# Optimization experiments

Hardware: AMD Instinct MI355X
Metric: run time of the kernel (lower is better)

Reference implementation:

```python
import jax, jax.numpy as jnp
import numpy as np

# Module config (init_kwargs)
OUT_H, OUT_W = 7, 7
SPATIAL_SCALE = 0.25
SAMPLE_NUM = 2          # fixed sampling grid (sample_num > 0 branch of mmcv kernel)
ALIGNED = True
CLOCKWISE = False

B, C, H, W = 2, 256, 200, 200
R = 1000


def setup_inputs() -> dict:
    key = jax.random.key(0)
    k1, k2, k3, k4, k5, k6 = jax.random.split(key, 6)
    features = jax.random.normal(k1, (B, C, H, W), dtype=jnp.float32)
    # rois: (batch_index, cx, cy, w, h, angle) in input-image coordinates
    bidx = jax.random.randint(k2, (R,), 0, B).astype(jnp.float32)
    cx = jax.random.uniform(k3, (R,), minval=100.0, maxval=700.0)
    cy = jax.random.uniform(k4, (R,), minval=100.0, maxval=700.0)
    wh = jax.random.uniform(k5, (R, 2), minval=20.0, maxval=200.0)
    ang = jax.random.uniform(k6, (R,), minval=-np.pi, maxval=np.pi)
    rois = jnp.concatenate(
        [bidx[:, None], cx[:, None], cy[:, None], wh, ang[:, None]], axis=1
    ).astype(jnp.float32)
    return {"features": features, "rois": rois}


def _bilinear_gather(features, bidx, y, x):
    """features: [B,C,H,W]; bidx: [R] int; y,x: [R,P] float. Returns [R,P,C]."""
    Hf, Wf = features.shape[2], features.shape[3]
    valid = (y > -1.0) & (y < Hf) & (x > -1.0) & (x < Wf)
    y = jnp.maximum(y, 0.0)
    x = jnp.maximum(x, 0.0)
    yl = jnp.floor(y).astype(jnp.int32)
    xl = jnp.floor(x).astype(jnp.int32)
    ych = yl >= Hf - 1
    xch = xl >= Wf - 1
    yl = jnp.where(ych, Hf - 1, yl)
    yh = jnp.where(ych, Hf - 1, yl + 1)
    xl = jnp.where(xch, Wf - 1, xl)
    xh = jnp.where(xch, Wf - 1, xl + 1)
    ly = jnp.where(ych, 0.0, y - yl.astype(y.dtype))
    lx = jnp.where(xch, 0.0, x - xl.astype(x.dtype))
    hy, hx = 1.0 - ly, 1.0 - lx
    b = bidx[:, None]  # [R,1] broadcast against [R,P]
    v1 = features[b, :, yl, xl]  # [R,P,C]
    v2 = features[b, :, yl, xh]
    v3 = features[b, :, yh, xl]
    v4 = features[b, :, yh, xh]
    val = (hy * hx)[..., None] * v1 + (hy * lx)[..., None] * v2 \
        + (ly * hx)[..., None] * v3 + (ly * lx)[..., None] * v4
    return jnp.where(valid[..., None], val, 0.0)


def _roi_align_rotated(features, rois):
    g = SAMPLE_NUM
    offset = 0.5 if ALIGNED else 0.0
    bidx = rois[:, 0].astype(jnp.int32)
    cx = rois[:, 1] * SPATIAL_SCALE - offset
    cy = rois[:, 2] * SPATIAL_SCALE - offset
    rw = rois[:, 3] * SPATIAL_SCALE
    rh = rois[:, 4] * SPATIAL_SCALE
    theta = -rois[:, 5] if CLOCKWISE else rois[:, 5]
    if not ALIGNED:
        rw = jnp.maximum(rw, 1.0)
        rh = jnp.maximum(rh, 1.0)
    bin_h = rh / OUT_H
    bin_w = rw / OUT_W
    # sample offsets within roi frame, origin at roi center
    ph = jnp.arange(OUT_H, dtype=jnp.float32)
    pw = jnp.arange(OUT_W, dtype=jnp.float32)
    ig = (jnp.arange(g, dtype=jnp.float32) + 0.5) / g
    # yy: [R, OUT_H, g]; xx: [R, OUT_W, g]
    yy = -rh[:, None, None] / 2.0 + (ph[None, :, None] + ig[None, None, :]) * bin_h[:, None, None]
    xx = -rw[:, None, None] / 2.0 + (pw[None, :, None] + ig[None, None, :]) * bin_w[:, None, None]
    # broadcast to [R, OUT_H, OUT_W, g, g]
    yy5 = yy[:, :, None, :, None]
    xx5 = xx[:, None, :, None, :]
    sin_t = jnp.sin(theta)[:, None, None, None, None]
    cos_t = jnp.cos(theta)[:, None, None, None, None]
    x = yy5 * sin_t + xx5 * cos_t + cx[:, None, None, None, None]
    y = yy5 * cos_t - xx5 * sin_t + cy[:, None, None, None, None]
    P = OUT_H * OUT_W * g * g
    vals = _bilinear_gather(features, bidx, y.reshape(R, P), x.reshape(R, P))  # [R,P,C]
    vals = vals.reshape(R, OUT_H, OUT_W, g * g, C).mean(axis=3)  # [R,OUT_H,OUT_W,C]
    return jnp.transpose(vals, (0, 3, 1, 2))  # [R,C,OUT_H,OUT_W]


def reference(features, rois):
    return _roi_align_rotated(features, rois)
```

## Files before the change

kernel.cpp:

```cpp
#include <hip/hip_runtime.h>
#include <math.h>

#define OUT_H 7
#define OUT_W 7
#define GS 2
#define NBINS (OUT_H * OUT_W)
#define NSAMP (GS * GS)
#define NMETA (NBINS * NSAMP)
#define SPATIAL_SCALE 0.25f
#define B_ 2
#define C_ 256
#define H_ 200
#define W_ 200
#define R_ 1000
#define HW_ (H_ * W_)

typedef _Float16 half_t;
typedef __attribute__((ext_vector_type(8))) _Float16 half8;
typedef __attribute__((ext_vector_type(2))) _Float16 half2_t;
typedef __attribute__((ext_vector_type(4))) float f32x4;


__global__ __launch_bounds__(256)
void nchw_to_nhwc_h(const float* __restrict__ in, half_t* __restrict__ out,
                    const float* __restrict__ rois, int* __restrict__ perm) {
    __shared__ float tile[64][64];

    __shared__ int bpos[8][64];
    __shared__ int novf, take;
    __shared__ unsigned char claimed[R_];
    __shared__ short ovf[R_];
    if (blockIdx.x == 0 && blockIdx.y == 0 && blockIdx.z == 0) {
        const int t0 = threadIdx.x;
        for (int i = t0; i < 8 * 64; i += 256) ((int*)bpos)[i] = 0;
        if (t0 == 0) { novf = 0; take = 0; }
        for (int t = t0; t < R_; t += 256) claimed[t] = 0;
        __syncthreads();
        for (int t = t0; t < R_; t += 256) {
            const float* roi = rois + t * 6;
            int   b   = (int)roi[0];
            float cyf = roi[2] * SPATIAL_SCALE;
            float cxf = roi[1] * SPATIAL_SCALE;
            int q = (int)((cyf - 25.0f) * (4.0f / 150.0f));
            q = q < 0 ? 0 : (q > 3 ? 3 : q);
            int band = b * 4 + q;
            band = band < 0 ? 0 : (band > 7 ? 7 : band);
            int bk = (int)((cxf - 25.0f) * (64.0f / 150.0f));
            bk = bk < 0 ? 0 : (bk > 63 ? 63 : bk);
            atomicAdd(&bpos[band][bk], 1);
        }
        __syncthreads();
        if (t0 < 8) {
            int s = 0;
            for (int k = 0; k < 64; ++k) {
                int c = bpos[t0][k];
                bpos[t0][k] = s;
                s += c;
            }
        }
        __syncthreads();
        for (int t = t0; t < R_; t += 256) {
            const float* roi = rois + t * 6;
            int   b   = (int)roi[0];
            float cyf = roi[2] * SPATIAL_SCALE;
            float cxf = roi[1] * SPATIAL_SCALE;
            int q = (int)((cyf - 25.0f) * (4.0f / 150.0f));
            q = q < 0 ? 0 : (q > 3 ? 3 : q);
            int band = b * 4 + q;
            band = band < 0 ? 0 : (band > 7 ? 7 : band);
            int bk = (int)((cxf - 25.0f) * (64.0f / 150.0f));
            bk = bk < 0 ? 0 : (bk > 63 ? 63 : bk);
            int pos = atomicAdd(&bpos[band][bk], 1);
            if (pos < R_ / 8) {
                int id = band + 8 * pos;
                perm[id] = t;
                claimed[id] = 1;
            } else {
                ovf[atomicAdd(&novf, 1)] = (short)t;
            }
        }
        __syncthreads();
        for (int t = t0; t < R_; t += 256) {
            if (!claimed[t]) perm[t] = (int)ovf[atomicAdd(&take, 1)];
        }
    }

    const int hw0 = blockIdx.x * 64;
    const int c0  = blockIdx.y * 64;
    const int b   = blockIdx.z;
    const int t   = threadIdx.x;

    {
        const f32x4* ip4 = (const f32x4*)(in + ((size_t)b * C_ + c0) * HW_ + hw0);
        const int r = t >> 4;
        const int q = t & 15;
#pragma unroll
        for (int k = 0; k < 4; ++k) {
            const int c = r + 16 * k;
            f32x4 v = __builtin_nontemporal_load(&ip4[(size_t)c * (HW_ / 4) + q]);
            const int g = q ^ ((c ^ (c >> 3)) & 7);
            ((f32x4*)tile)[c * 16 + g] = v;
        }
    }
    __syncthreads();
    {
        const int cg = t & 7;
        const int hb = t >> 3;
        half_t* op = out + ((size_t)b * HW_ + hw0) * C_ + c0 + 8 * cg;
#pragma unroll
        for (int i = 0; i < 2; ++i) {
            const int hw = hb + 32 * i;
            const int gh = hw >> 2, oh = hw & 3;
            half8 h;
#pragma unroll
            for (int dc = 0; dc < 8; ++dc) {
                const int c = 8 * cg + dc;
                const float f = tile[c][4 * (gh ^ ((c ^ (c >> 3)) & 7)) + oh];
                h[dc] = (half_t)f;
            }
            *(half8*)(op + (size_t)hw * C_) = h;
        }
    }
}

__device__ __forceinline__ void mix2(float& a0, float& a1,
                                     unsigned int pair, float w) {
    asm("v_fma_mix_f32 %0, %1, %2, %0 op_sel:[0,0,0] op_sel_hi:[1,0,0]"
        : "+v"(a0) : "v"(pair), "v"(w));
    asm("v_fma_mix_f32 %0, %1, %2, %0 op_sel:[1,0,0] op_sel_hi:[1,0,0]"
        : "+v"(a1) : "v"(pair), "v"(w));
}

struct Taps { uint2 t[16]; };

__device__ __forceinline__ void load_taps(Taps& T, const uint2* __restrict__ fpu,
                                          const int4* __restrict__ s_o,
                                          int m, int lane) {
#pragma unroll
    for (int i = 0; i < 4; ++i) {
        const int4 o = s_o[m + i];
        T.t[4 * i + 0] = fpu[o.x + lane];
        T.t[4 * i + 1] = fpu[o.y + lane];
        T.t[4 * i + 2] = fpu[o.z + lane];
        T.t[4 * i + 3] = fpu[o.w + lane];
    }
}

__device__ __forceinline__ void fma_store(const Taps& T,
                                          const float4* __restrict__ s_w,
                                          int m, int j, int lane,
                                          float (&obuf)[4][64][NBINS]) {
    float ax = 0.0f, ay = 0.0f, az = 0.0f, aw = 0.0f;
#pragma unroll
    for (int i = 0; i < 4; ++i) {
        const float4 w = s_w[m + i];
        mix2(ax, ay, T.t[4 * i + 0].x, w.x); mix2(az, aw, T.t[4 * i + 0].y, w.x);
        mix2(ax, ay, T.t[4 * i + 1].x, w.y); mix2(az, aw, T.t[4 * i + 1].y, w.y);
        mix2(ax, ay, T.t[4 * i + 2].x, w.z); mix2(az, aw, T.t[4 * i + 2].y, w.z);
        mix2(ax, ay, T.t[4 * i + 3].x, w.w); mix2(az, aw, T.t[4 * i + 3].y, w.w);
    }
    obuf[0][lane][j] = ax;
    obuf[1][lane][j] = ay;
    obuf[2][lane][j] = az;
    obuf[3][lane][j] = aw;
}

__global__ __launch_bounds__(512, 4)
void gather_nhwc(const half_t* __restrict__ nhwc,
                 const float* __restrict__ rois,
                 const int* __restrict__ perm,
                 float* __restrict__ out) {
    __shared__ float  obuf[4][64][NBINS];
    __shared__ int4   s_o[NMETA];
    __shared__ float4 s_w[NMETA];

    const int r    = perm[blockIdx.x];
    const int tid  = threadIdx.x;
    const int wave = tid >> 6;
    const int lane = tid & 63;

    if (tid < NMETA) {
        const float* roi = rois + r * 6;
        const int   b     = (int)roi[0];
        const float cx    = roi[1] * SPATIAL_SCALE - 0.5f;
        const float cy    = roi[2] * SPATIAL_SCALE - 0.5f;
        const float rw    = roi[3] * SPATIAL_SCALE;
        const float rh    = roi[4] * SPATIAL_SCALE;
        const float theta = roi[5];
        const float bin_h = rh * (1.0f / OUT_H);
        const float bin_w = rw * (1.0f / OUT_W);
        float st, ct;
        __sincosf(theta, &st, &ct);

        const int bin = tid >> 2;
        const int s   = tid & 3;
        const int ph  = bin / OUT_W, pw = bin % OUT_W;
        const int iy  = s >> 1,      ix = s & 1;

        const float yy = -rh * 0.5f + ((float)ph + ((float)iy + 0.5f) * 0.5f) * bin_h;
        const float xx = -rw * 0.5f + ((float)pw + ((float)ix + 0.5f) * 0.5f) * bin_w;
        float x = yy * st + xx * ct + cx;
        float y = yy * ct - xx * st + cy;

        const bool valid = (y > -1.0f) && (y < (float)H_) &&
                           (x > -1.0f) && (x < (float)W_);
        y = fmaxf(y, 0.0f);
        x = fmaxf(x, 0.0f);
        int yl = (int)y, xl = (int)x;
        int yh; float ly;
        if (yl >= H_ - 1) { yl = H_ - 1; yh = H_ - 1; ly = 0.0f; }
        else              { yh = yl + 1; ly = y - (float)yl; }
        int xh; float lx;
        if (xl >= W_ - 1) { xl = W_ - 1; xh = W_ - 1; lx = 0.0f; }
        else              { xh = xl + 1; lx = x - (float)xl; }
        const float hy = 1.0f - ly, hx = 1.0f - lx;
        const float scale = valid ? (1.0f / NSAMP) : 0.0f;

        const int bplane = b * HW_;
        s_o[tid] = make_int4((bplane + yl * W_ + xl) * (C_ / 4),
                             (bplane + yl * W_ + xh) * (C_ / 4),
                             (bplane + yh * W_ + xl) * (C_ / 4),
                             (bplane + yh * W_ + xh) * (C_ / 4));
        s_w[tid] = make_float4(hy * hx * scale, hy * lx * scale,
                               ly * hx * scale, ly * lx * scale);
    }
    __syncthreads();

    const uint2* __restrict__ fpu = (const uint2*)nhwc;

    {
        Taps A, B;
        int jA = wave;
        int jB = wave + 8;
        load_taps(A, fpu, s_o, 4 * jA, lane);
        if (jB < NBINS) load_taps(B, fpu, s_o, 4 * jB, lane);
        __builtin_amdgcn_sched_barrier(0);

        fma_store(A, s_w, 4 * jA, jA, lane, obuf);
        jA += 16;
        if (jA < NBINS) load_taps(A, fpu, s_o, 4 * jA, lane);
        __builtin_amdgcn_sched_barrier(0);
        if (jB < NBINS) {
            fma_store(B, s_w, 4 * jB, jB, lane, obuf);
            jB += 16;
            if (jB < NBINS) load_taps(B, fpu, s_o, 4 * jB, lane);
            __builtin_amdgcn_sched_barrier(0);
        }
        if (jA < NBINS) {
            fma_store(A, s_w, 4 * jA, jA, lane, obuf);
            jA += 16;
            if (jA < NBINS) load_taps(A, fpu, s_o, 4 * jA, lane);
            __builtin_amdgcn_sched_barrier(0);
        }
        if (jB < NBINS) {
            fma_store(B, s_w, 4 * jB, jB, lane, obuf);
            jB += 16;
            if (jB < NBINS) load_taps(B, fpu, s_o, 4 * jB, lane);
            __builtin_amdgcn_sched_barrier(0);
        }
        if (jA < NBINS) {
            fma_store(A, s_w, 4 * jA, jA, lane, obuf);
            jA += 16;
            if (jA < NBINS) load_taps(A, fpu, s_o, 4 * jA, lane);
            __builtin_amdgcn_sched_barrier(0);
        }
        if (jB < NBINS) {
            fma_store(B, s_w, 4 * jB, jB, lane, obuf);
            jB += 16;
        }
        if (jA < NBINS) {
            fma_store(A, s_w, 4 * jA, jA, lane, obuf);
        }
    }
    __syncthreads();

    float* out_r = out + (size_t)r * (C_ * NBINS);
    const int E = C_ * NBINS;
#pragma unroll
    for (int i = 0; i < (E + 511) / 512; ++i) {
        const int f = tid + 512 * i;
        if (f < E) {
            const int c = f / NBINS;
            const int j = f - c * NBINS;
            __builtin_nontemporal_store(obuf[c & 3][c >> 2][j], &out_r[f]);
        }
    }
}


struct alignas(16) Samp {
    int o0, o1, o2, o3;
    float w0, w1, w2, w3;
};

__device__ __forceinline__ Samp compute_samp(const float* __restrict__ rois,
                                             int r, int ph, int pw, int s) {
    const float* roi = rois + r * 6;
    int   b     = (int)roi[0];
    float cx    = roi[1] * SPATIAL_SCALE - 0.5f;
    float cy    = roi[2] * SPATIAL_SCALE - 0.5f;
    float rw    = roi[3] * SPATIAL_SCALE;
    float rh    = roi[4] * SPATIAL_SCALE;
    float theta = roi[5];
    float bin_h = rh * (1.0f / OUT_H);
    float bin_w = rw * (1.0f / OUT_W);
    int iy = s / GS, ix = s % GS;
    float yy = -rh * 0.5f + ((float)ph + ((float)iy + 0.5f) * (1.0f / GS)) * bin_h;
    float xx = -rw * 0.5f + ((float)pw + ((float)ix + 0.5f) * (1.0f / GS)) * bin_w;
    float st = sinf(theta), ct = cosf(theta);
    float x = yy * st + xx * ct + cx;
    float y = yy * ct - xx * st + cy;
    bool valid = (y > -1.0f) && (y < (float)H_) && (x > -1.0f) && (x < (float)W_);
    y = fmaxf(y, 0.0f);
    x = fmaxf(x, 0.0f);
    int yl = (int)y;
    int xl = (int)x;
    int yh; float ly;
    if (yl >= H_ - 1) { yl = H_ - 1; yh = H_ - 1; ly = 0.0f; }
    else              { yh = yl + 1; ly = y - (float)yl; }
    int xh; float lx;
    if (xl >= W_ - 1) { xl = W_ - 1; xh = W_ - 1; lx = 0.0f; }
    else              { xh = xl + 1; lx = x - (float)xl; }
    float hy = 1.0f - ly, hx = 1.0f - lx;
    float scale = valid ? (1.0f / NSAMP) : 0.0f;
    Samp sp;
    int base = b * (C_ * H_ * W_);
    sp.o0 = base + yl * W_ + xl;
    sp.o1 = base + yl * W_ + xh;
    sp.o2 = base + yh * W_ + xl;
    sp.o3 = base + yh * W_ + xh;
    sp.w0 = hy * hx * scale;
    sp.w1 = hy * lx * scale;
    sp.w2 = ly * hx * scale;
    sp.w3 = ly * lx * scale;
    return sp;
}

__global__ __launch_bounds__(256)
void mono_kernel(const float* __restrict__ feat,
                 const float* __restrict__ rois,
                 float* __restrict__ out) {
    int tid = blockIdx.x * blockDim.x + threadIdx.x;
    if (tid >= R_ * C_ * NBINS) return;
    int bin = tid % NBINS;
    int rc  = tid / NBINS;
    int c   = rc % C_;
    int r   = rc / C_;
    int coff = c * (H_ * W_);
    float acc = 0.0f;
#pragma unroll
    for (int s = 0; s < NSAMP; ++s) {
        Samp t = compute_samp(rois, r, bin / OUT_W, bin % OUT_W, s);
        acc += t.w0 * feat[coff + t.o0];
        acc += t.w1 * feat[coff + t.o1];
        acc += t.w2 * feat[coff + t.o2];
        acc += t.w3 * feat[coff + t.o3];
    }
    out[tid] = acc;
}


extern "C" void kernel_launch(void* const* d_in, const int* in_sizes, int n_in,
                              void* d_out, int out_size, void* d_ws, size_t ws_size,
                              hipStream_t stream) {
    const float* feat = (const float*)d_in[0];
    const float* rois = (const float*)d_in[1];
    float* out = (float*)d_out;

    const size_t nhwc_bytes = (size_t)B_ * C_ * HW_ * sizeof(half_t);
    const size_t perm_bytes = (size_t)R_ * sizeof(int);

    if (ws_size >= nhwc_bytes + perm_bytes) {
        half_t* nhwc = (half_t*)d_ws;
        int*    perm = (int*)((char*)d_ws + nhwc_bytes);
        dim3 tgrid(HW_ / 64, C_ / 64, B_);
        nchw_to_nhwc_h<<<tgrid, 256, 0, stream>>>(feat, nhwc, rois, perm);
        gather_nhwc<<<R_, 512, 0, stream>>>(nhwc, rois, perm, out);
    } else {
        const int n_out = R_ * C_ * NBINS;
        mono_kernel<<<(n_out + 255) / 256, 256, 0, stream>>>(feat, rois, out);
    }
}
```

Baseline: 157.9 us.

## Load horizontally adjacent bilinear taps as one contiguous 16-byte pair per lane

In NHWC half layout the xl and xh taps sit in adjacent pixels, so each lane now reads a 16-byte uint4 covering 8 channels. The lower half-wave reads the left pixel and the upper half-wave reads the right one, which cuts the number of gather load instructions per sample from four to two. The right-edge case is remapped to xp=W-2 with weights (0,1) so the pair load stays in bounds. The two half-waves' partial sums are combined with a cross-lane shuffle, and the shared output buffer is re-laid out as 8 channels by 32 lanes. This adds shuffles and halves the number of lanes doing stores in exchange for fewer, wider memory requests.

```diff
diff --git a/kernel.cpp b/kernel.cpp
--- a/kernel.cpp
+++ b/kernel.cpp
@@ -131,38 +131,42 @@
         : "+v"(a1) : "v"(pair), "v"(w));
 }
 
-struct Taps { uint2 t[16]; };
-
-__device__ __forceinline__ void load_taps(Taps& T, const uint2* __restrict__ fpu,
-                                          const int4* __restrict__ s_o,
-                                          int m, int lane) {
-#pragma unroll
-    for (int i = 0; i < 4; ++i) {
-        const int4 o = s_o[m + i];
-        T.t[4 * i + 0] = fpu[o.x + lane];
-        T.t[4 * i + 1] = fpu[o.y + lane];
-        T.t[4 * i + 2] = fpu[o.z + lane];
-        T.t[4 * i + 3] = fpu[o.w + lane];
-    }
-}
-
-__device__ __forceinline__ void fma_store(const Taps& T,
+__device__ __forceinline__ void mix8(float (&a)[8], const uint4& t, float w) {
+    mix2(a[0], a[1], t.x, w); mix2(a[2], a[3], t.y, w);
+    mix2(a[4], a[5], t.z, w); mix2(a[6], a[7], t.w, w);
+}
+
+struct TapsP { uint4 t[8]; };
+
+__device__ __forceinline__ void load_pairs(TapsP& T, const uint4* __restrict__ fp4,
+                                           const int2* __restrict__ s_o,
+                                           int m, int lane) {
+#pragma unroll
+    for (int s = 0; s < 4; ++s) {
+        const int2 o = s_o[m + s];
+        T.t[2 * s + 0] = fp4[o.x + lane];
+        T.t[2 * s + 1] = fp4[o.y + lane];
+    }
+}
+
+__device__ __forceinline__ void fma_store(const TapsP& T,
                                           const float4* __restrict__ s_w,
                                           int m, int j, int lane,
-                                          float (&obuf)[4][64][NBINS]) {
-    float ax = 0.0f, ay = 0.0f, az = 0.0f, aw = 0.0f;
-#pragma unroll
-    for (int i = 0; i < 4; ++i) {
-        const float4 w = s_w[m + i];
-        mix2(ax, ay, T.t[4 * i + 0].x, w.x); mix2(az, aw, T.t[4 * i + 0].y, w.x);
-        mix2(ax, ay, T.t[4 * i + 1].x, w.y); mix2(az, aw, T.t[4 * i + 1].y, w.y);
-        mix2(ax, ay, T.t[4 * i + 2].x, w.z); mix2(az, aw, T.t[4 * i + 2].y, w.z);
-        mix2(ax, ay, T.t[4 * i + 3].x, w.w); mix2(az, aw, T.t[4 * i + 3].y, w.w);
-    }
-    obuf[0][lane][j] = ax;
-    obuf[1][lane][j] = ay;
-    obuf[2][lane][j] = az;
-    obuf[3][lane][j] = aw;
+                                          float (&obuf)[8][32][NBINS]) {
+    float a[8] = {0.f, 0.f, 0.f, 0.f, 0.f, 0.f, 0.f, 0.f};
+    const float2* w2 = ((const float2*)s_w) + (lane >> 5);
+#pragma unroll
+    for (int s = 0; s < 4; ++s) {
+        const float2 ws = w2[2 * (m + s)];
+        mix8(a, T.t[2 * s + 0], ws.x);
+        mix8(a, T.t[2 * s + 1], ws.y);
+    }
+#pragma unroll
+    for (int k = 0; k < 8; ++k) a[k] += __shfl_xor(a[k], 32, 64);
+    if (lane < 32) {
+#pragma unroll
+        for (int k = 0; k < 8; ++k) obuf[k][lane][j] = a[k];
+    }
 }
 
 __global__ __launch_bounds__(512, 4)
@@ -170,8 +174,8 @@
                  const float* __restrict__ rois,
                  const int* __restrict__ perm,
                  float* __restrict__ out) {
-    __shared__ float  obuf[4][64][NBINS];
-    __shared__ int4   s_o[NMETA];
+    __shared__ float  obuf[8][32][NBINS];
+    __shared__ int2   s_o[NMETA];
     __shared__ float4 s_w[NMETA];
 
     const int r    = perm[blockIdx.x];
@@ -210,58 +214,57 @@
         int yh; float ly;
         if (yl >= H_ - 1) { yl = H_ - 1; yh = H_ - 1; ly = 0.0f; }
         else              { yh = yl + 1; ly = y - (float)yl; }
-        int xh; float lx;
-        if (xl >= W_ - 1) { xl = W_ - 1; xh = W_ - 1; lx = 0.0f; }
-        else              { xh = xl + 1; lx = x - (float)xl; }
-        const float hy = 1.0f - ly, hx = 1.0f - lx;
+        int xp; float e0, e1;
+        if (xl >= W_ - 1) { xp = W_ - 2; e0 = 0.0f; e1 = 1.0f; }
+        else              { xp = xl; const float lx = x - (float)xl;
+                            e0 = 1.0f - lx; e1 = lx; }
+        const float hy = 1.0f - ly;
         const float scale = valid ? (1.0f / NSAMP) : 0.0f;
 
         const int bplane = b * HW_;
-        s_o[tid] = make_int4((bplane + yl * W_ + xl) * (C_ / 4),
-                             (bplane + yl * W_ + xh) * (C_ / 4),
-                             (bplane + yh * W_ + xl) * (C_ / 4),
-                             (bplane + yh * W_ + xh) * (C_ / 4));
-        s_w[tid] = make_float4(hy * hx * scale, hy * lx * scale,
-                               ly * hx * scale, ly * lx * scale);
+        s_o[tid] = make_int2((bplane + yl * W_ + xp) * 32,
+                             (bplane + yh * W_ + xp) * 32);
+        s_w[tid] = make_float4(hy * e0 * scale, ly * e0 * scale,
+                               hy * e1 * scale, ly * e1 * scale);
     }
     __syncthreads();
 
-    const uint2* __restrict__ fpu = (const uint2*)nhwc;
+    const uint4* __restrict__ fp4 = (const uint4*)nhwc;
 
     {
-        Taps A, B;
+        TapsP A, B;
         int jA = wave;
         int jB = wave + 8;
-        load_taps(A, fpu, s_o, 4 * jA, lane);
-        if (jB < NBINS) load_taps(B, fpu, s_o, 4 * jB, lane);
+        load_pairs(A, fp4, s_o, 4 * jA, lane);
+        if (jB < NBINS) load_pairs(B, fp4, s_o, 4 * jB, lane);
         __builtin_amdgcn_sched_barrier(0);
 
         fma_store(A, s_w, 4 * jA, jA, lane, obuf);
         jA += 16;
-        if (jA < NBINS) load_taps(A, fpu, s_o, 4 * jA, lane);
+        if (jA < NBINS) load_pairs(A, fp4, s_o, 4 * jA, lane);
         __builtin_amdgcn_sched_barrier(0);
         if (jB < NBINS) {
             fma_store(B, s_w, 4 * jB, jB, lane, obuf);
             jB += 16;
-            if (jB < NBINS) load_taps(B, fpu, s_o, 4 * jB, lane);
+            if (jB < NBINS) load_pairs(B, fp4, s_o, 4 * jB, lane);
             __builtin_amdgcn_sched_barrier(0);
         }
         if (jA < NBINS) {
             fma_store(A, s_w, 4 * jA, jA, lane, obuf);
             jA += 16;
-            if (jA < NBINS) load_taps(A, fpu, s_o, 4 * jA, lane);
+            if (jA < NBINS) load_pairs(A, fp4, s_o, 4 * jA, lane);
             __builtin_amdgcn_sched_barrier(0);
         }
         if (jB < NBINS) {
             fma_store(B, s_w, 4 * jB, jB, lane, obuf);
             jB += 16;
-            if (jB < NBINS) load_taps(B, fpu, s_o, 4 * jB, lane);
+            if (jB < NBINS) load_pairs(B, fp4, s_o, 4 * jB, lane);
             __builtin_amdgcn_sched_barrier(0);
         }
         if (jA < NBINS) {
             fma_store(A, s_w, 4 * jA, jA, lane, obuf);
             jA += 16;
-            if (jA < NBINS) load_taps(A, fpu, s_o, 4 * jA, lane);
+            if (jA < NBINS) load_pairs(A, fp4, s_o, 4 * jA, lane);
             __builtin_amdgcn_sched_barrier(0);
         }
         if (jB < NBINS) {
@@ -282,7 +285,7 @@
         if (f < E) {
             const int c = f / NBINS;
             const int j = f - c * NBINS;
-            __builtin_nontemporal_store(obuf[c & 3][c >> 2][j], &out_r[f]);
+            __builtin_nontemporal_store(obuf[c & 7][c >> 3][j], &out_r[f]);
         }
     }
 }
```

After: 151.6 us (median of 2 runs). -4.0%, faster.
